# Kernel optimization log

Measured on AMD Instinct MI355X. Metric: run time of the kernel, lower is better.

## Reference

```python
import jax, jax.numpy as jnp
import numpy as np


def setup_inputs() -> dict:
    key = jax.random.key(0)
    k1, k2, k3 = jax.random.split(key, 3)
    B, L, I, H = 128, 1024, 256, 512
    x = jax.random.normal(k1, (B, L, I), dtype=jnp.float32)
    h0 = jnp.zeros((B, H), dtype=jnp.float32)
    # scale like nn.Linear default-ish init to keep tanh non-saturated
    Wx = jax.random.normal(k2, (I, H), dtype=jnp.float32) * (1.0 / np.sqrt(I))
    bx = jnp.zeros((H,), dtype=jnp.float32)
    Wh = jax.random.normal(k3, (H, H), dtype=jnp.float32) * (1.0 / np.sqrt(H))
    bh = jnp.zeros((H,), dtype=jnp.float32)
    return {"x": x, "h0": h0, "Wx": Wx, "bx": bx, "Wh": Wh, "bh": bh}


def reference(x, h0, Wx, bx, Wh, bh):
    # Precompute input projections for all timesteps in one big GEMM: [B,L,H]
    x_proj = jnp.einsum("bli,ih->blh", x, Wx) + bx

    def step(h, xp_t):  # h: [B,H], xp_t: [B,H]
        h_new = jnp.tanh(xp_t + h @ Wh + bh)
        return h_new, h_new

    # scan over time axis; outputs stacked as [L, B, H] matching torch.stack(results)
    _, hs = jax.lax.scan(step, h0, jnp.swapaxes(x_proj, 0, 1))
    return hs
```

## Files before the change

### kernel.cpp

```cpp
#include <hip/hip_runtime.h>
#include <cstdint>
#include <cmath>

#define BB 128
#define LL 1024
#define II 256
#define HH 512

typedef _Float16 f16;
typedef _Float16 f16x2 __attribute__((ext_vector_type(2)));
typedef _Float16 f16x4 __attribute__((ext_vector_type(4)));
typedef _Float16 f16x8 __attribute__((ext_vector_type(8)));
typedef float f32x4 __attribute__((ext_vector_type(4)));

__global__ __launch_bounds__(256, 4) void xproj_gemm(
    const float* __restrict__ x, const float* __restrict__ Wx,
    const float* __restrict__ bx, float* __restrict__ out) {
  const int t0 = blockIdx.x;
  const int n0 = blockIdx.y * 128;
  __shared__ f16 As[128][72];
  __shared__ f16 Bs[128][72];
  const int tid  = threadIdx.x;
  const int lane = tid & 63;
  const int wid  = tid >> 6;
  const int wr   = wid >> 1, wc = wid & 1;

  f32x4 acc[4][4];
#pragma unroll
  for (int mi = 0; mi < 4; ++mi)
#pragma unroll
    for (int ni = 0; ni < 4; ++ni) acc[mi][ni] = f32x4{0.f, 0.f, 0.f, 0.f};

  for (int kt = 0; kt < 4; ++kt) {
    const int k0 = kt * 64;
#pragma unroll
    for (int rep = 0; rep < 8; ++rep) {
      const int idx = rep * 256 + tid;
      const int row = idx >> 4;
      const int c4  = idx & 15;
      const float4 v =
          *(reinterpret_cast<const float4*>(x + ((size_t)row * LL + t0) * II + k0) + c4);
      f16x4 p = {(f16)v.x, (f16)v.y, (f16)v.z, (f16)v.w};
      *reinterpret_cast<f16x4*>(&As[row][c4 * 4]) = p;
    }
    {
      const int c  = tid & 127;
      const int kh = tid >> 7;
      const float* wp = Wx + (size_t)(k0 + kh * 32) * HH + n0 + c;
#pragma unroll
      for (int m8 = 0; m8 < 4; ++m8) {
        f16x8 pk;
#pragma unroll
        for (int j = 0; j < 8; ++j) pk[j] = (f16)wp[(size_t)(m8 * 8 + j) * HH];
        *reinterpret_cast<f16x8*>(&Bs[c][kh * 32 + m8 * 8]) = pk;
      }
    }
    __syncthreads();
#pragma unroll
    for (int kk2 = 0; kk2 < 2; ++kk2) {
      const int kf = kk2 * 32 + ((lane >> 4) << 3);
      f16x8 af[4], bf[4];
#pragma unroll
      for (int mi = 0; mi < 4; ++mi)
        af[mi] = *reinterpret_cast<const f16x8*>(&As[wr * 64 + mi * 16 + (lane & 15)][kf]);
#pragma unroll
      for (int ni = 0; ni < 4; ++ni)
        bf[ni] = *reinterpret_cast<const f16x8*>(&Bs[wc * 64 + ni * 16 + (lane & 15)][kf]);
#pragma unroll
      for (int mi = 0; mi < 4; ++mi)
#pragma unroll
        for (int ni = 0; ni < 4; ++ni)
          acc[mi][ni] =
              __builtin_amdgcn_mfma_f32_16x16x32_f16(af[mi], bf[ni], acc[mi][ni], 0, 0, 0);
    }
    __syncthreads();
  }
#pragma unroll
  for (int mi = 0; mi < 4; ++mi) {
    const int row = wr * 64 + mi * 16 + ((lane >> 4) << 2);
#pragma unroll
    for (int ni = 0; ni < 4; ++ni) {
      const int col = n0 + wc * 64 + ni * 16 + (lane & 15);
      const float bxi = bx[col];
#pragma unroll
      for (int q = 0; q < 4; ++q)
        out[((size_t)t0 * BB + (row + q)) * HH + col] = acc[mi][ni][q] + bxi;
    }
  }
}

#define SMEM_BYTES 140288

__device__ __forceinline__ float fdot2(uint32_t w, uint32_t h, float acc) {
#if __has_builtin(__builtin_amdgcn_fdot2)
  return __builtin_amdgcn_fdot2(__builtin_bit_cast(f16x2, w),
                                __builtin_bit_cast(f16x2, h), acc, false);
#else
  asm("v_dot2_f32_f16 %0, %1, %2, %0" : "+v"(acc) : "v"(w), "v"(h));
  return acc;
#endif
}

__global__ __launch_bounds__(1024, 4) void rnn_scan(
    const float* __restrict__ Wh, const float* __restrict__ bh,
    const float* __restrict__ h0, float* __restrict__ out) {
  extern __shared__ unsigned char smem[];
  uint32_t* wlds = reinterpret_cast<uint32_t*>(smem);
  uint32_t* hpk  = reinterpret_cast<uint32_t*>(smem + 131072);
  float*    red  = reinterpret_cast<float*>(smem + 132096);

  const int r   = blockIdx.x;
  const int tid = threadIdx.x;
  const int j2  = tid & 255;
  const int kq  = tid >> 8;
  const int c0  = j2 * 2;
  const int kbase = kq * 128;
  const int sw  = (tid & 7) << 2;

  uint32_t wreg[96];
#pragma unroll
  for (int p = 0; p < 64; ++p) {
    const int k = kbase + 2 * p;
    const float2 lo = *reinterpret_cast<const float2*>(Wh + (size_t)k * HH + c0);
    const float2 hi = *reinterpret_cast<const float2*>(Wh + (size_t)(k + 1) * HH + c0);
    f16x2 p0 = {(f16)lo.x, (f16)hi.x};
    f16x2 p1 = {(f16)lo.y, (f16)hi.y};
    const uint32_t u0 = __builtin_bit_cast(uint32_t, p0);
    const uint32_t u1 = __builtin_bit_cast(uint32_t, p1);
    if (p < 48) {
      wreg[2 * p]     = u0;
      wreg[2 * p + 1] = u1;
    } else {
      const int l0 = 2 * (p - 48);
      wlds[tid * 32 + (l0 ^ sw)]       = u0;
      wlds[tid * 32 + ((l0 + 1) ^ sw)] = u1;
    }
  }
  const float bh_r = (tid < HH) ? bh[tid] : 0.f;
  if (tid < 256) {
    f16x2 hp = {(f16)h0[(size_t)r * HH + 2 * tid], (f16)h0[(size_t)r * HH + 2 * tid + 1]};
    hpk[tid] = __builtin_bit_cast(uint32_t, hp);
  }
  __syncthreads();

  const int hbase = kq * 64;
  float* orow = out + (size_t)r * HH;
  for (int t = 0; t < LL; ++t) {
    const float xpv = orow[(size_t)t * (BB * HH) + (tid & 511)];
    float a0 = 0.f, a1 = 0.f;
    const uint32_t* hp = hpk + hbase;
#pragma unroll
    for (int u = 0; u < 12; ++u) {
      const uint4 hv = *reinterpret_cast<const uint4*>(hp + 4 * u);
      a0 = fdot2(wreg[8 * u + 0], hv.x, a0); a1 = fdot2(wreg[8 * u + 1], hv.x, a1);
      a0 = fdot2(wreg[8 * u + 2], hv.y, a0); a1 = fdot2(wreg[8 * u + 3], hv.y, a1);
      a0 = fdot2(wreg[8 * u + 4], hv.z, a0); a1 = fdot2(wreg[8 * u + 5], hv.z, a1);
      a0 = fdot2(wreg[8 * u + 6], hv.w, a0); a1 = fdot2(wreg[8 * u + 7], hv.w, a1);
    }
#pragma unroll
    for (int u = 0; u < 8; ++u) {
      const uint4 wv = *reinterpret_cast<const uint4*>(wlds + tid * 32 + ((4 * u) ^ sw));
      const uint2 hv = *reinterpret_cast<const uint2*>(hp + 48 + 2 * u);
      a0 = fdot2(wv.x, hv.x, a0); a1 = fdot2(wv.y, hv.x, a1);
      a0 = fdot2(wv.z, hv.y, a0); a1 = fdot2(wv.w, hv.y, a1);
    }
    *reinterpret_cast<float2*>(red + kq * HH + c0) = make_float2(a0, a1);
    __syncthreads();
    if (tid < HH) {
      const float s = red[tid] + red[HH + tid] + red[2 * HH + tid] + red[3 * HH + tid] +
                      xpv + bh_r;
      const float h = tanhf(s);
      orow[(size_t)t * (BB * HH) + tid] = h;
      const float hn = __shfl_down(h, 1, 64);
      if (!(tid & 1)) {
        f16x2 hp2 = {(f16)h, (f16)hn};
        hpk[tid >> 1] = __builtin_bit_cast(uint32_t, hp2);
      }
    }
    __syncthreads();
  }
}

extern "C" void kernel_launch(void* const* d_in, const int* in_sizes, int n_in,
                              void* d_out, int out_size, void* d_ws, size_t ws_size,
                              hipStream_t stream) {
  const float* x  = (const float*)d_in[0];
  const float* h0 = (const float*)d_in[1];
  const float* Wx = (const float*)d_in[2];
  const float* bx = (const float*)d_in[3];
  const float* Wh = (const float*)d_in[4];
  const float* bh = (const float*)d_in[5];
  float* out = (float*)d_out;

  (void)in_sizes; (void)n_in; (void)out_size; (void)d_ws; (void)ws_size;

  hipFuncSetAttribute(reinterpret_cast<const void*>(rnn_scan),
                      hipFuncAttributeMaxDynamicSharedMemorySize, SMEM_BYTES);

  xproj_gemm<<<dim3(LL, HH / 128), 256, 0, stream>>>(x, Wx, bx, out);
  rnn_scan<<<dim3(BB), 1024, SMEM_BYTES, stream>>>(Wh, bh, h0, out);
}
```

Measured before the change: 2.228 ms.

## Restructure RNN scan to 512 threads with 4 columns per thread

The recurrent scan kernel drops from 1024 to 512 threads per block. Each thread now computes 4 output columns over a 128-wide K slice and keeps 208 packed fp16 weight words in registers (the rest in LDS), raising register-held weight reuse per h load. It also double-buffers the hidden state, prefetches the next timestep's input projection, and swaps tanhf for an exp2/rcp approximation. The cost is higher register pressure, which the waves_per_eu attribute is meant to constrain, and slightly lower tanh accuracy.

```diff
diff --git a/kernel.cpp b/kernel.cpp
--- a/kernel.cpp
+++ b/kernel.cpp
@@ -1,6 +1,5 @@
 #include <hip/hip_runtime.h>
 #include <cstdint>
-#include <cmath>
 
 #define BB 128
 #define LL 1024
@@ -89,7 +88,9 @@
   }
 }
 
-#define SMEM_BYTES 140288
+#define RP 52
+#define WSTRIDE 64
+#define SMEM_BYTES (131072 + 1024 + 1024 + 8192)
 
 __device__ __forceinline__ float fdot2(uint32_t w, uint32_t h, float acc) {
 #if __has_builtin(__builtin_amdgcn_fdot2)
@@ -101,83 +102,120 @@
 #endif
 }
 
-__global__ __launch_bounds__(1024, 4) void rnn_scan(
-    const float* __restrict__ Wh, const float* __restrict__ bh,
-    const float* __restrict__ h0, float* __restrict__ out) {
+__device__ __forceinline__ float fast_tanh(float s) {
+  const float z = 2.885390081777927f * s;
+#if __has_builtin(__builtin_amdgcn_exp2f)
+  const float e = __builtin_amdgcn_exp2f(z);
+#else
+  const float e = __builtin_exp2f(z);
+#endif
+#if __has_builtin(__builtin_amdgcn_rcpf)
+  return 1.f - 2.f * __builtin_amdgcn_rcpf(e + 1.f);
+#else
+  return 1.f - 2.f / (e + 1.f);
+#endif
+}
+
+__global__ __launch_bounds__(512)
+__attribute__((amdgpu_waves_per_eu(2, 2)))
+void rnn_scan(const float* __restrict__ Wh, const float* __restrict__ bh,
+              const float* __restrict__ h0, float* __restrict__ out) {
   extern __shared__ unsigned char smem[];
   uint32_t* wlds = reinterpret_cast<uint32_t*>(smem);
-  uint32_t* hpk  = reinterpret_cast<uint32_t*>(smem + 131072);
-  float*    red  = reinterpret_cast<float*>(smem + 132096);
+  uint32_t* hA   = reinterpret_cast<uint32_t*>(smem + 131072);
+  uint32_t* hB   = reinterpret_cast<uint32_t*>(smem + 132096);
+  float*    red  = reinterpret_cast<float*>(smem + 133120);
 
   const int r   = blockIdx.x;
   const int tid = threadIdx.x;
-  const int j2  = tid & 255;
-  const int kq  = tid >> 8;
-  const int c0  = j2 * 2;
-  const int kbase = kq * 128;
+  const int kq  = tid >> 7;
+  const int c0  = (tid & 127) * 4;
+  const int kb  = kq * 128;
   const int sw  = (tid & 7) << 2;
 
-  uint32_t wreg[96];
+  uint32_t wreg[4 * RP];
 #pragma unroll
   for (int p = 0; p < 64; ++p) {
-    const int k = kbase + 2 * p;
-    const float2 lo = *reinterpret_cast<const float2*>(Wh + (size_t)k * HH + c0);
-    const float2 hi = *reinterpret_cast<const float2*>(Wh + (size_t)(k + 1) * HH + c0);
-    f16x2 p0 = {(f16)lo.x, (f16)hi.x};
-    f16x2 p1 = {(f16)lo.y, (f16)hi.y};
-    const uint32_t u0 = __builtin_bit_cast(uint32_t, p0);
-    const uint32_t u1 = __builtin_bit_cast(uint32_t, p1);
-    if (p < 48) {
-      wreg[2 * p]     = u0;
-      wreg[2 * p + 1] = u1;
+    const float4 r0 = *reinterpret_cast<const float4*>(Wh + (size_t)(kb + 2 * p) * HH + c0);
+    const float4 r1 = *reinterpret_cast<const float4*>(Wh + (size_t)(kb + 2 * p + 1) * HH + c0);
+    f16x2 q0 = {(f16)r0.x, (f16)r1.x};
+    f16x2 q1 = {(f16)r0.y, (f16)r1.y};
+    f16x2 q2 = {(f16)r0.z, (f16)r1.z};
+    f16x2 q3 = {(f16)r0.w, (f16)r1.w};
+    const uint32_t d0 = __builtin_bit_cast(uint32_t, q0);
+    const uint32_t d1 = __builtin_bit_cast(uint32_t, q1);
+    const uint32_t d2 = __builtin_bit_cast(uint32_t, q2);
+    const uint32_t d3 = __builtin_bit_cast(uint32_t, q3);
+    if (p < RP) {
+      wreg[4 * p + 0] = d0; wreg[4 * p + 1] = d1;
+      wreg[4 * p + 2] = d2; wreg[4 * p + 3] = d3;
     } else {
-      const int l0 = 2 * (p - 48);
-      wlds[tid * 32 + (l0 ^ sw)]       = u0;
-      wlds[tid * 32 + ((l0 + 1) ^ sw)] = u1;
-    }
-  }
-  const float bh_r = (tid < HH) ? bh[tid] : 0.f;
+      uint4 w4 = {d0, d1, d2, d3};
+      *reinterpret_cast<uint4*>(wlds + tid * WSTRIDE + ((4 * (p - RP)) ^ sw)) = w4;
+    }
+  }
+  const float bh_r = bh[tid];
   if (tid < 256) {
     f16x2 hp = {(f16)h0[(size_t)r * HH + 2 * tid], (f16)h0[(size_t)r * HH + 2 * tid + 1]};
-    hpk[tid] = __builtin_bit_cast(uint32_t, hp);
-  }
+    hA[tid] = __builtin_bit_cast(uint32_t, hp);
+  }
+  float* orow = out + (size_t)r * HH;
+  float xpv = orow[tid];
   __syncthreads();
 
-  const int hbase = kq * 64;
-  float* orow = out + (size_t)r * HH;
+  uint32_t* hcur = hA;
+  uint32_t* hnxt = hB;
+#pragma unroll 1
   for (int t = 0; t < LL; ++t) {
-    const float xpv = orow[(size_t)t * (BB * HH) + (tid & 511)];
-    float a0 = 0.f, a1 = 0.f;
-    const uint32_t* hp = hpk + hbase;
-#pragma unroll
-    for (int u = 0; u < 12; ++u) {
-      const uint4 hv = *reinterpret_cast<const uint4*>(hp + 4 * u);
-      a0 = fdot2(wreg[8 * u + 0], hv.x, a0); a1 = fdot2(wreg[8 * u + 1], hv.x, a1);
-      a0 = fdot2(wreg[8 * u + 2], hv.y, a0); a1 = fdot2(wreg[8 * u + 3], hv.y, a1);
-      a0 = fdot2(wreg[8 * u + 4], hv.z, a0); a1 = fdot2(wreg[8 * u + 5], hv.z, a1);
-      a0 = fdot2(wreg[8 * u + 6], hv.w, a0); a1 = fdot2(wreg[8 * u + 7], hv.w, a1);
-    }
-#pragma unroll
-    for (int u = 0; u < 8; ++u) {
-      const uint4 wv = *reinterpret_cast<const uint4*>(wlds + tid * 32 + ((4 * u) ^ sw));
-      const uint2 hv = *reinterpret_cast<const uint2*>(hp + 48 + 2 * u);
-      a0 = fdot2(wv.x, hv.x, a0); a1 = fdot2(wv.y, hv.x, a1);
-      a0 = fdot2(wv.z, hv.y, a0); a1 = fdot2(wv.w, hv.y, a1);
-    }
-    *reinterpret_cast<float2*>(red + kq * HH + c0) = make_float2(a0, a1);
-    __syncthreads();
-    if (tid < HH) {
-      const float s = red[tid] + red[HH + tid] + red[2 * HH + tid] + red[3 * HH + tid] +
-                      xpv + bh_r;
-      const float h = tanhf(s);
-      orow[(size_t)t * (BB * HH) + tid] = h;
-      const float hn = __shfl_down(h, 1, 64);
-      if (!(tid & 1)) {
-        f16x2 hp2 = {(f16)h, (f16)hn};
-        hpk[tid >> 1] = __builtin_bit_cast(uint32_t, hp2);
+    const int tn = (t + 1 < LL) ? t + 1 : LL - 1;
+    const float xpv_n = orow[(size_t)tn * (BB * HH) + tid];
+
+    float a0 = 0.f, a1 = 0.f, a2 = 0.f, a3 = 0.f;
+    const uint4* hc4 = reinterpret_cast<const uint4*>(hcur) + kq * 16;
+#pragma unroll
+    for (int u = 0; u < 13; ++u) {
+      const uint4 hv = hc4[u];
+      const uint32_t hs[4] = {hv.x, hv.y, hv.z, hv.w};
+#pragma unroll
+      for (int e = 0; e < 4; ++e) {
+        const int p = 4 * u + e;
+        a0 = fdot2(wreg[4 * p + 0], hs[e], a0);
+        a1 = fdot2(wreg[4 * p + 1], hs[e], a1);
+        a2 = fdot2(wreg[4 * p + 2], hs[e], a2);
+        a3 = fdot2(wreg[4 * p + 3], hs[e], a3);
       }
     }
-    __syncthreads();
+#pragma unroll
+    for (int u = 13; u < 16; ++u) {
+      const uint4 hv = hc4[u];
+      const uint32_t hs[4] = {hv.x, hv.y, hv.z, hv.w};
+#pragma unroll
+      for (int e = 0; e < 4; ++e) {
+        const int p = 4 * u + e;
+        const uint4 wv =
+            *reinterpret_cast<const uint4*>(wlds + tid * WSTRIDE + ((4 * (p - RP)) ^ sw));
+        a0 = fdot2(wv.x, hs[e], a0);
+        a1 = fdot2(wv.y, hs[e], a1);
+        a2 = fdot2(wv.z, hs[e], a2);
+        a3 = fdot2(wv.w, hs[e], a3);
+      }
+    }
+    *reinterpret_cast<f32x4*>(red + kq * HH + c0) = f32x4{a0, a1, a2, a3};
+    __syncthreads();
+
+    const float s =
+        red[tid] + red[HH + tid] + red[2 * HH + tid] + red[3 * HH + tid] + xpv + bh_r;
+    const float h = fast_tanh(s);
+    orow[(size_t)t * (BB * HH) + tid] = h;
+    const float hn = __shfl_down(h, 1, 64);
+    if (!(tid & 1)) {
+      f16x2 hp2 = {(f16)h, (f16)hn};
+      hnxt[tid >> 1] = __builtin_bit_cast(uint32_t, hp2);
+    }
+    __syncthreads();
+
+    uint32_t* tmp = hcur; hcur = hnxt; hnxt = tmp;
+    xpv = xpv_n;
   }
 }
 
@@ -198,5 +236,5 @@
                       hipFuncAttributeMaxDynamicSharedMemorySize, SMEM_BYTES);
 
   xproj_gemm<<<dim3(LL, HH / 128), 256, 0, stream>>>(x, Wx, bx, out);
-  rnn_scan<<<dim3(BB), 1024, SMEM_BYTES, stream>>>(Wh, bh, h0, out);
-}
+  rnn_scan<<<dim3(BB), 512, SMEM_BYTES, stream>>>(Wh, bh, h0, out);
+}
```

After: 2.331 ms. +4.6%, slower.
